# Kernel tuning notes

Measured on AMD Instinct MI355X. Metric: run time of the kernel, lower is better.

## Reference

```python
import jax, jax.numpy as jnp
import numpy as np

NUM_USERS = 150000
NUM_ITEMS = 140000
NUM_BRANDS = 10000
N_NODES = NUM_USERS + NUM_ITEMS + NUM_BRANDS
EMBED_DIM = 64
N_LAYERS = 3
N_EDGES = 1200000


def setup_inputs() -> dict:
    key = jax.random.key(0)
    k1, k2, k3, k4, k5, k6 = jax.random.split(key, 6)
    # Xavier-uniform-ish init scale for embeddings
    s = float(np.sqrt(6.0 / (N_NODES + EMBED_DIM)))
    user_emb = jax.random.normal(k1, (NUM_USERS, EMBED_DIM), dtype=jnp.float32) * s
    item_emb = jax.random.normal(k2, (NUM_ITEMS, EMBED_DIM), dtype=jnp.float32) * s
    brand_emb = jax.random.normal(k3, (NUM_BRANDS, EMBED_DIM), dtype=jnp.float32) * s
    edge_src = jax.random.randint(k4, (N_EDGES,), 0, N_NODES, dtype=jnp.int32)
    edge_dst = jax.random.randint(k5, (N_EDGES,), 0, N_NODES, dtype=jnp.int32)
    # symmetric-normalized-adjacency-like positive values
    edge_vals = jax.random.uniform(k6, (N_EDGES,), dtype=jnp.float32)
    return {
        "user_emb": user_emb,
        "item_emb": item_emb,
        "brand_emb": brand_emb,
        "edge_vals": edge_vals,
        "edge_src": edge_src,
        "edge_dst": edge_dst,
    }


def _spmm(edge_src, edge_dst, edge_vals, x):
    # out[d] = sum_{e: dst[e]=d} vals[e] * x[src[e]]  (COO SpMM)
    msgs = x[edge_src] * edge_vals[:, None]  # [E, D]
    return jax.ops.segment_sum(msgs, edge_dst, num_segments=N_NODES)


def reference(user_emb, item_emb, brand_emb, edge_vals, edge_src, edge_dst):
    ego = jnp.concatenate([user_emb, item_emb, brand_emb], axis=0)  # [N, D]
    acc = ego
    h = ego
    for _ in range(N_LAYERS):
        h = _spmm(edge_src, edge_dst, edge_vals, h)
        acc = acc + h
    final = acc / jnp.float32(N_LAYERS + 1)  # mean over layer stack
    final_user = final[:NUM_USERS]
    final_item = final[NUM_USERS:NUM_USERS + NUM_ITEMS]
    return (final_user, final_item)
```

## Files before the change

### kernel.cpp

```cpp
#include <hip/hip_runtime.h>

#define NUM_USERS  150000
#define NUM_ITEMS  140000
#define NUM_BRANDS 10000
#define N_NODES    300000
#define DIM        64
#define N_EDGES    1200000
#define OUT_ROWS   290000

#define CHUNK      1024
#define NB         ((N_NODES + CHUNK - 1) / CHUNK)

#define NBIN       8
#define BINSZ      (N_EDGES / NBIN)

__device__ __forceinline__ float bf_lo(unsigned u) { return __uint_as_float(u << 16); }
__device__ __forceinline__ float bf_hi(unsigned u) { return __uint_as_float(u & 0xffff0000u); }
__device__ __forceinline__ unsigned pack_bf(float a, float b) {
    unsigned ua = __float_as_uint(a); ua += 0x7fffu + ((ua >> 16) & 1u);
    unsigned ub = __float_as_uint(b); ub += 0x7fffu + ((ub >> 16) & 1u);
    return (ua >> 16) | (ub & 0xffff0000u);
}

__global__ void lgcn_hist(const int* __restrict__ dst,
                          int* __restrict__ counts,
                          int* __restrict__ rank) {
    int e = blockIdx.x * blockDim.x + threadIdx.x;
    if (e >= N_EDGES) return;
    rank[e] = atomicAdd(&counts[dst[e]], 1);
}

__global__ void lgcn_scan_p1(const int* __restrict__ counts,
                             int* __restrict__ rowptr,
                             int* __restrict__ blockSums) {
    __shared__ int ts[256];
    int b    = blockIdx.x;
    int base = b * CHUNK;
    int t    = threadIdx.x;
    int c[4];
    int s = 0;
#pragma unroll
    for (int i = 0; i < 4; ++i) {
        int g = base + t * 4 + i;
        c[i] = (g < N_NODES) ? counts[g] : 0;
        s += c[i];
    }
    ts[t] = s;
    __syncthreads();
    for (int off = 1; off < 256; off <<= 1) {
        int v = (t >= off) ? ts[t - off] : 0;
        __syncthreads();
        ts[t] += v;
        __syncthreads();
    }
    int run = ts[t] - s;
#pragma unroll
    for (int i = 0; i < 4; ++i) {
        int g = base + t * 4 + i;
        if (g < N_NODES) rowptr[g] = run;
        run += c[i];
    }
    if (t == 255) blockSums[b] = ts[255];
}

__global__ void lgcn_scan_p2(int* __restrict__ blockSums) {
    __shared__ int sh[512];
    int t = threadIdx.x;
    int v = (t < NB) ? blockSums[t] : 0;
    sh[t] = v;
    __syncthreads();
    for (int off = 1; off < 512; off <<= 1) {
        int u = (t >= off) ? sh[t - off] : 0;
        __syncthreads();
        sh[t] += u;
        __syncthreads();
    }
    if (t < NB) blockSums[t] = sh[t] - v;
}

__global__ void lgcn_scan_p3(int* __restrict__ rowptr,
                             const int* __restrict__ blockSums) {
    int b    = blockIdx.x;
    int base = b * CHUNK;
    int t    = threadIdx.x;
    int off  = blockSums[b];
#pragma unroll
    for (int i = 0; i < 4; ++i) {
        int g = base + t * 4 + i;
        if (g < N_NODES) rowptr[g] += off;
    }
    if (b == 0 && t == 0) rowptr[N_NODES] = N_EDGES;
}

__global__ void lgcn_csr_bin(const int*   __restrict__ src,
                             const int*   __restrict__ dst,
                             const float* __restrict__ vals,
                             const int*   __restrict__ rank,
                             const int*   __restrict__ rowptr,
                             uint2*       __restrict__ csr) {
    int b    = blockIdx.x;
    int bin  = b & (NBIN - 1);
    int e    = (b >> 3) * blockDim.x + threadIdx.x;
    if (e >= N_EDGES) return;
    int pos = rowptr[dst[e]] + rank[e];
    int lo  = bin * BINSZ;
    if (pos >= lo && pos < lo + BINSZ) {
        uint2 rec;
        rec.x = (unsigned)src[e];
        rec.y = __float_as_uint(vals[e]);
        csr[pos] = rec;
    }
}

__device__ __forceinline__ const float4* ego_row(const float* __restrict__ user,
                                                 const float* __restrict__ item,
                                                 const float* __restrict__ brand,
                                                 int r) {
    if (r < NUM_USERS)
        return reinterpret_cast<const float4*>(user) + (r << 4);
    else if (r < NUM_USERS + NUM_ITEMS)
        return reinterpret_cast<const float4*>(item) + ((r - NUM_USERS) << 4);
    else
        return reinterpret_cast<const float4*>(brand) + ((r - NUM_USERS - NUM_ITEMS) << 4);
}

template <int LAYER>
__device__ __forceinline__ void load8(const float* __restrict__ user,
                                      const float* __restrict__ item,
                                      const float* __restrict__ brand,
                                      const uint4* __restrict__ h_src,
                                      int r, int q, float4& a, float4& b) {
    if (LAYER == 1) {
        const float4* er = ego_row(user, item, brand, r);
        a = er[2 * q];
        b = er[2 * q + 1];
    } else {
        uint4 w = h_src[(r << 3) + q];
        a = make_float4(bf_lo(w.x), bf_hi(w.x), bf_lo(w.y), bf_hi(w.y));
        b = make_float4(bf_lo(w.z), bf_hi(w.z), bf_lo(w.w), bf_hi(w.w));
    }
}

template <int LAYER>
__global__ void lgcn_gather(const int*   __restrict__ rowptr,
                            const uint2* __restrict__ csr,
                            const float* __restrict__ user,
                            const float* __restrict__ item,
                            const float* __restrict__ brand,
                            const uint4* __restrict__ h1,
                            const uint4* __restrict__ h2,
                            uint4*       __restrict__ h_out,
                            float*       __restrict__ out) {
    int t    = blockIdx.x * blockDim.x + threadIdx.x;
    int node = t >> 3;
    int q    = t & 7;
    int beg = rowptr[node];
    int end = rowptr[node + 1];
    const uint4* h_src = (LAYER == 2) ? h1 : h2;
    float4 s0 = make_float4(0.f, 0.f, 0.f, 0.f);
    float4 s1 = make_float4(0.f, 0.f, 0.f, 0.f);
    if (beg < end) {
        uint2 rec0 = csr[beg];
        uint2 rec1 = csr[(beg + 1 < end) ? beg + 1 : beg];
        float4 a0, b0;
        load8<LAYER>(user, item, brand, h_src, (int)rec0.x, q, a0, b0);
        for (int j = beg; j < end; ++j) {
            int jn = j + 2 < end ? j + 2 : end - 1;
            uint2 rec2 = csr[jn];
            float4 a1, b1;
            load8<LAYER>(user, item, brand, h_src, (int)rec1.x, q, a1, b1);
            float v = __uint_as_float(rec0.y);
            s0.x = fmaf(a0.x, v, s0.x);
            s0.y = fmaf(a0.y, v, s0.y);
            s0.z = fmaf(a0.z, v, s0.z);
            s0.w = fmaf(a0.w, v, s0.w);
            s1.x = fmaf(b0.x, v, s1.x);
            s1.y = fmaf(b0.y, v, s1.y);
            s1.z = fmaf(b0.z, v, s1.z);
            s1.w = fmaf(b0.w, v, s1.w);
            rec0 = rec1; rec1 = rec2; a0 = a1; b0 = b1;
        }
    }
    if (LAYER != 3) {
        uint4 w;
        w.x = pack_bf(s0.x, s0.y);
        w.y = pack_bf(s0.z, s0.w);
        w.z = pack_bf(s1.x, s1.y);
        w.w = pack_bf(s1.z, s1.w);
        h_out[t] = w;
    } else if (node < OUT_ROWS) {
        const float4* er = ego_row(user, item, brand, node);
        float4 e0 = er[2 * q];
        float4 e1 = er[2 * q + 1];
        uint4 w1 = h1[t];
        uint4 w2 = h2[t];
        float4 o0, o1;
        o0.x = (e0.x + bf_lo(w1.x) + bf_lo(w2.x) + s0.x) * 0.25f;
        o0.y = (e0.y + bf_hi(w1.x) + bf_hi(w2.x) + s0.y) * 0.25f;
        o0.z = (e0.z + bf_lo(w1.y) + bf_lo(w2.y) + s0.z) * 0.25f;
        o0.w = (e0.w + bf_hi(w1.y) + bf_hi(w2.y) + s0.w) * 0.25f;
        o1.x = (e1.x + bf_lo(w1.z) + bf_lo(w2.z) + s1.x) * 0.25f;
        o1.y = (e1.y + bf_hi(w1.z) + bf_hi(w2.z) + s1.y) * 0.25f;
        o1.z = (e1.z + bf_lo(w1.w) + bf_lo(w2.w) + s1.z) * 0.25f;
        o1.w = (e1.w + bf_hi(w1.w) + bf_hi(w2.w) + s1.w) * 0.25f;
        float4* o = reinterpret_cast<float4*>(out) + t * 2;
        o[0] = o0;
        o[1] = o1;
    }
}

extern "C" void kernel_launch(void* const* d_in, const int* in_sizes, int n_in,
                              void* d_out, int out_size, void* d_ws, size_t ws_size,
                              hipStream_t stream) {
    const float* user  = (const float*)d_in[0];
    const float* item  = (const float*)d_in[1];
    const float* brand = (const float*)d_in[2];
    const float* vals  = (const float*)d_in[3];
    const int*   src   = (const int*)d_in[4];
    const int*   dst   = (const int*)d_in[5];
    float* out = (float*)d_out;

    size_t W = 0;
    uint4* h1  = (uint4*)d_ws;                 W += (size_t)N_NODES * 32;
    uint4* h2  = (uint4*)((int*)d_ws + W);     W += (size_t)N_NODES * 32;
    uint2* csr = (uint2*)((int*)d_ws + W);     W += (size_t)N_EDGES * 2;
    int* rank      = (int*)d_ws + W;           W += N_EDGES;
    int* rowptr    = (int*)d_ws + W;           W += N_NODES + 2;
    int* counts    = (int*)d_ws + W;           W += N_NODES;
    int* blockSums = (int*)d_ws + W;           W += 512;
    (void)ws_size; (void)n_in; (void)in_sizes; (void)out_size;

    const int edgeBlocks   = (N_EDGES + 255) / 256;
    const int gatherBlocks = (N_NODES * 8) / 256;

    hipMemsetAsync(counts, 0, (size_t)N_NODES * sizeof(int), stream);

    lgcn_hist   <<<edgeBlocks, 256, 0, stream>>>(dst, counts, rank);
    lgcn_scan_p1<<<NB, 256, 0, stream>>>(counts, rowptr, blockSums);
    lgcn_scan_p2<<<1, 512, 0, stream>>>(blockSums);
    lgcn_scan_p3<<<NB, 256, 0, stream>>>(rowptr, blockSums);
    lgcn_csr_bin<<<NBIN * edgeBlocks, 256, 0, stream>>>(src, dst, vals, rank,
                                                        rowptr, csr);

    lgcn_gather<1><<<gatherBlocks, 256, 0, stream>>>(rowptr, csr, user, item, brand,
                                                     h1, h2, h1, out);
    lgcn_gather<2><<<gatherBlocks, 256, 0, stream>>>(rowptr, csr, user, item, brand,
                                                     h1, h2, h2, out);
    lgcn_gather<3><<<gatherBlocks, 256, 0, stream>>>(rowptr, csr, user, item, brand,
                                                     h1, h2, nullptr, out);
}
```

Measured before the change: 261.4 us.

## Replace 8-pass binned CSR scatter with two-pass partition then fill

The old CSR build launched 8x the edge blocks, and every pass re-read dst/rank/rowptr/src/vals to scatter only the edges landing in one position bin. The new code partitions edges once into per-bin staging buckets using shared-memory counters and a global per-bin cursor, storing src, val and target position. A second kernel then scatters each bin's records into the CSR, keeping writes localized per bin. This removes the redundant reads at the cost of an extra 16-byte-per-edge staging buffer and one more launch. The cursor is zeroed by widening the existing memset, which relies on cursor8 sitting directly after counts.

```diff
diff --git a/kernel.cpp b/kernel.cpp
--- a/kernel.cpp
+++ b/kernel.cpp
@@ -92,24 +92,45 @@
     if (b == 0 && t == 0) rowptr[N_NODES] = N_EDGES;
 }
 
-__global__ void lgcn_csr_bin(const int*   __restrict__ src,
-                             const int*   __restrict__ dst,
-                             const float* __restrict__ vals,
-                             const int*   __restrict__ rank,
-                             const int*   __restrict__ rowptr,
-                             uint2*       __restrict__ csr) {
-    int b    = blockIdx.x;
-    int bin  = b & (NBIN - 1);
-    int e    = (b >> 3) * blockDim.x + threadIdx.x;
-    if (e >= N_EDGES) return;
-    int pos = rowptr[dst[e]] + rank[e];
-    int lo  = bin * BINSZ;
-    if (pos >= lo && pos < lo + BINSZ) {
-        uint2 rec;
+__global__ void lgcn_part(const int*   __restrict__ src,
+                          const int*   __restrict__ dst,
+                          const float* __restrict__ vals,
+                          const int*   __restrict__ rank,
+                          const int*   __restrict__ rowptr,
+                          int*         __restrict__ cursor8,
+                          uint4*       __restrict__ binBuf) {
+    __shared__ int cnt[NBIN];
+    __shared__ int base[NBIN];
+    int t = threadIdx.x;
+    int e = blockIdx.x * blockDim.x + t;
+    if (t < NBIN) cnt[t] = 0;
+    __syncthreads();
+    int bin = 0, lr = 0;
+    uint4 rec;
+    bool valid = (e < N_EDGES);
+    if (valid) {
+        int pos = rowptr[dst[e]] + rank[e];
+        bin = pos / BINSZ;
+        lr  = atomicAdd(&cnt[bin], 1);
         rec.x = (unsigned)src[e];
         rec.y = __float_as_uint(vals[e]);
-        csr[pos] = rec;
-    }
+        rec.z = (unsigned)pos;
+        rec.w = 0;
+    }
+    __syncthreads();
+    if (t < NBIN) base[t] = atomicAdd(&cursor8[t], cnt[t]);
+    __syncthreads();
+    if (valid) binBuf[(size_t)bin * BINSZ + base[bin] + lr] = rec;
+}
+
+__global__ void lgcn_fill(const uint4* __restrict__ binBuf,
+                          uint2*       __restrict__ csr) {
+    int b   = blockIdx.x;
+    int bin = b & (NBIN - 1);
+    int i   = (b >> 3) * blockDim.x + threadIdx.x;
+    if (i >= BINSZ) return;
+    uint4 rec = binBuf[(size_t)bin * BINSZ + i];
+    csr[rec.z] = make_uint2(rec.x, rec.y);
 }
 
 __device__ __forceinline__ const float4* ego_row(const float* __restrict__ user,
@@ -224,23 +245,27 @@
     uint4* h1  = (uint4*)d_ws;                 W += (size_t)N_NODES * 32;
     uint4* h2  = (uint4*)((int*)d_ws + W);     W += (size_t)N_NODES * 32;
     uint2* csr = (uint2*)((int*)d_ws + W);     W += (size_t)N_EDGES * 2;
+    uint4* binBuf = (uint4*)((int*)d_ws + W);  W += (size_t)N_EDGES * 4;
     int* rank      = (int*)d_ws + W;           W += N_EDGES;
     int* rowptr    = (int*)d_ws + W;           W += N_NODES + 2;
     int* counts    = (int*)d_ws + W;           W += N_NODES;
+    int* cursor8   = (int*)d_ws + W;           W += 16;
     int* blockSums = (int*)d_ws + W;           W += 512;
     (void)ws_size; (void)n_in; (void)in_sizes; (void)out_size;
 
     const int edgeBlocks   = (N_EDGES + 255) / 256;
+    const int fillBlocks   = NBIN * ((BINSZ + 255) / 256);
     const int gatherBlocks = (N_NODES * 8) / 256;
 
-    hipMemsetAsync(counts, 0, (size_t)N_NODES * sizeof(int), stream);
+    hipMemsetAsync(counts, 0, (size_t)(N_NODES + 16) * sizeof(int), stream);
 
     lgcn_hist   <<<edgeBlocks, 256, 0, stream>>>(dst, counts, rank);
     lgcn_scan_p1<<<NB, 256, 0, stream>>>(counts, rowptr, blockSums);
     lgcn_scan_p2<<<1, 512, 0, stream>>>(blockSums);
     lgcn_scan_p3<<<NB, 256, 0, stream>>>(rowptr, blockSums);
-    lgcn_csr_bin<<<NBIN * edgeBlocks, 256, 0, stream>>>(src, dst, vals, rank,
-                                                        rowptr, csr);
+    lgcn_part   <<<edgeBlocks, 256, 0, stream>>>(src, dst, vals, rank, rowptr,
+                                                 cursor8, binBuf);
+    lgcn_fill   <<<fillBlocks, 256, 0, stream>>>(binBuf, csr);
 
     lgcn_gather<1><<<gatherBlocks, 256, 0, stream>>>(rowptr, csr, user, item, brand,
                                                      h1, h2, h1, out);
```

After: 278.0 us. 6.4% more time.
